# Optimization experiments

Hardware: AMD Instinct MI355X
Metric: run time of the kernel (lower is better)

Reference implementation:

```python
import jax, jax.numpy as jnp
import numpy as np

LATENT = 128
DISC = 64
RNN = 512
CODE = 512
INPUT = 2


def _lstm_cell(x, h, c, Wih, Whh, bih, bhh):
    # PyTorch LSTMCell: gate order (i, f, g, o)
    gates = x @ Wih.T + h @ Whh.T + bih + bhh
    i, f, g, o = jnp.split(gates, 4, axis=-1)
    c_new = jax.nn.sigmoid(f) * c + jax.nn.sigmoid(i) * jnp.tanh(g)
    h_new = jax.nn.sigmoid(o) * jnp.tanh(c_new)
    return h_new, c_new


def setup_inputs() -> dict:
    key = jax.random.key(0)
    ks = jax.random.split(key, 12)
    B = 4096
    s = lambda *sh: 1.0 / np.sqrt(sh[-1])
    inp = {
        'latent': jax.random.normal(ks[0], (B, LATENT), dtype=jnp.float32),
        'W_unpack': jax.random.normal(ks[1], (CODE, LATENT + INPUT), dtype=jnp.float32) * s(CODE, LATENT + INPUT),
        'b_unpack': jnp.zeros((CODE,), dtype=jnp.float32),
        'Wih0': jax.random.normal(ks[2], (4 * RNN, CODE), dtype=jnp.float32) * s(4 * RNN, CODE),
        'Whh0': jax.random.normal(ks[3], (4 * RNN, RNN), dtype=jnp.float32) * s(4 * RNN, RNN),
        'bih0': jnp.zeros((4 * RNN,), dtype=jnp.float32),
        'bhh0': jnp.zeros((4 * RNN,), dtype=jnp.float32),
        'Wih1': jax.random.normal(ks[4], (4 * RNN, RNN), dtype=jnp.float32) * s(4 * RNN, RNN),
        'Whh1': jax.random.normal(ks[5], (4 * RNN, RNN), dtype=jnp.float32) * s(4 * RNN, RNN),
        'bih1': jnp.zeros((4 * RNN,), dtype=jnp.float32),
        'bhh1': jnp.zeros((4 * RNN,), dtype=jnp.float32),
        'W_angle': jax.random.normal(ks[6], (DISC, RNN), dtype=jnp.float32) * s(DISC, RNN),
        'b_angle': jnp.zeros((DISC,), dtype=jnp.float32),
        'num_segments': 64,
    }
    return inp


def reference(latent, W_unpack, b_unpack, Wih0, Whh0, bih0, bhh0,
              Wih1, Whh1, bih1, bhh1, W_angle, b_angle, num_segments):
    B = latent.shape[0]
    space = jnp.linspace(-1.0, 1.0, DISC, dtype=latent.dtype)  # [DISC]
    # fixed gumbel noise for all steps: [S, B, DISC]
    u = jax.random.uniform(jax.random.key(42), (num_segments, B, DISC),
                           dtype=latent.dtype, minval=1e-8, maxval=1.0)
    gumbels = -jnp.log(-jnp.log(u))

    def step(carry, g):
        prev, h0, c0, h1, c1 = carry
        x = jnp.tanh(jnp.concatenate([latent, prev], axis=-1) @ W_unpack.T + b_unpack)
        h0, c0 = _lstm_cell(x, h0, c0, Wih0, Whh0, bih0, bhh0)
        h1, c1 = _lstm_cell(h0, h1, c1, Wih1, Whh1, bih1, bhh1)
        logits = h1 @ W_angle.T + b_angle
        # gumbel-softmax, tau=1 (torch default), hard=True with straight-through
        y_soft = jax.nn.softmax(logits + g, axis=-1)
        y_hard = jax.nn.one_hot(jnp.argmax(y_soft, axis=-1), DISC, dtype=y_soft.dtype)
        y = y_soft + jax.lax.stop_gradient(y_hard - y_soft)
        angles = jnp.sum(y * space, axis=-1, keepdims=True)  # [B,1]
        seg = jnp.concatenate([angles, jnp.zeros_like(angles)], axis=-1)  # [B,2]
        return (seg, h0, c0, h1, c1), seg

    z = jnp.zeros((B, RNN), dtype=latent.dtype)
    init = (jnp.zeros((B, INPUT), dtype=latent.dtype), z, z, z, z)
    _, segs = jax.lax.scan(step, init, gumbels)  # [S, B, 2]
    return jnp.transpose(segs, (1, 0, 2))  # [B, S, 2]
```

## Files before the change

kernel.cpp:

```cpp
#include <hip/hip_runtime.h>
#include <cstdint>

#define BATCH 4096
#define LATENT 128
#define RNN 512
#define CODE 512
#define DISC 64
#define NSEG 64
#define UNPACK_COLS 130

__device__ __forceinline__ uint32_t rotl32(uint32_t x, uint32_t r) {
  return (x << r) | (x >> (32u - r));
}

__device__ __forceinline__ uint32_t threefry_bits(uint32_t n) {
  const uint32_t k0 = 0u, k1 = 42u;
  const uint32_t ks2 = k0 ^ k1 ^ 0x1BD11BDAu;
  uint32_t x0 = 0u, x1 = n;
  x0 += k0; x1 += k1;
#define TF_ROUND(r) { x0 += x1; x1 = rotl32(x1, r); x1 ^= x0; }
  TF_ROUND(13) TF_ROUND(15) TF_ROUND(26) TF_ROUND(6)
  x0 += k1;  x1 += ks2 + 1u;
  TF_ROUND(17) TF_ROUND(29) TF_ROUND(16) TF_ROUND(24)
  x0 += ks2; x1 += k0 + 2u;
  TF_ROUND(13) TF_ROUND(15) TF_ROUND(26) TF_ROUND(6)
  x0 += k0;  x1 += k1 + 3u;
  TF_ROUND(17) TF_ROUND(29) TF_ROUND(16) TF_ROUND(24)
  x0 += k1;  x1 += ks2 + 4u;
  TF_ROUND(13) TF_ROUND(15) TF_ROUND(26) TF_ROUND(6)
  x0 += ks2; x1 += k0 + 5u;
#undef TF_ROUND
  return x0 ^ x1;
}

__global__ __launch_bounds__(256) void base_kernel(
    const float* __restrict__ latent, const float* __restrict__ Wu,
    const float* __restrict__ bu, float* __restrict__ base) {
  __shared__ float lrow[LATENT];
  const int b = blockIdx.x;
  if (threadIdx.x < LATENT) lrow[threadIdx.x] = latent[b * LATENT + threadIdx.x];
  __syncthreads();
  for (int n = threadIdx.x; n < CODE; n += 256) {
    const float* wr = Wu + (size_t)n * UNPACK_COLS;
    float acc = 0.f;
#pragma unroll 8
    for (int k = 0; k < LATENT; ++k) acc += lrow[k] * wr[k];
    base[(size_t)b * CODE + n] = acc + bu[n];
  }
}

__global__ __launch_bounds__(256) void x_kernel(
    const float* __restrict__ base, const float* __restrict__ angle,
    const float* __restrict__ Wu, float* __restrict__ xo) {
  const int idx = blockIdx.x * 256 + threadIdx.x;
  const int b = idx >> 9;
  const int n = idx & 511;
  xo[idx] = tanhf(base[idx] + angle[b] * Wu[(size_t)n * UNPACK_COLS + 128]);
}

#define BM 128
#define BN 128
#define BK 16

__global__ __launch_bounds__(256) void gemm_dual(
    const float* __restrict__ A1, const float* __restrict__ W1,
    const float* __restrict__ A2, const float* __restrict__ W2,
    const float* __restrict__ b1, const float* __restrict__ b2,
    float* __restrict__ C) {
  const int K = RNN;
  const int N = 4 * RNN;
  __shared__ __align__(16) float As[BK][BM];
  __shared__ __align__(16) float Ws[BK][BN];
  const int tid = threadIdx.x;
  const int tx = tid & 15, ty = tid >> 4;
  const int rowBase = blockIdx.y * BM;
  const int colBase = blockIdx.x * BN;
  const int lrow = tid >> 2;
  const int lk = (tid & 3) * 4;

  float acc[8][8];
#pragma unroll
  for (int i = 0; i < 8; ++i)
#pragma unroll
    for (int j = 0; j < 8; ++j) acc[i][j] = 0.f;

  for (int seg = 0; seg < 2; ++seg) {
    const float* __restrict__ A = seg ? A2 : A1;
    const float* __restrict__ W = seg ? W2 : W1;
    for (int k0 = 0; k0 < K; k0 += BK) {
      __syncthreads();
#pragma unroll
      for (int r = 0; r < 2; ++r) {
        const int rr = lrow + r * 64;
        float4 va = *(const float4*)&A[(size_t)(rowBase + rr) * K + k0 + lk];
        As[lk + 0][rr] = va.x; As[lk + 1][rr] = va.y;
        As[lk + 2][rr] = va.z; As[lk + 3][rr] = va.w;
        float4 vw = *(const float4*)&W[(size_t)(colBase + rr) * K + k0 + lk];
        Ws[lk + 0][rr] = vw.x; Ws[lk + 1][rr] = vw.y;
        Ws[lk + 2][rr] = vw.z; Ws[lk + 3][rr] = vw.w;
      }
      __syncthreads();
#pragma unroll
      for (int kk = 0; kk < BK; ++kk) {
        float4 a0 = *(const float4*)&As[kk][ty * 8];
        float4 a1 = *(const float4*)&As[kk][ty * 8 + 4];
        float4 w0 = *(const float4*)&Ws[kk][tx * 8];
        float4 w1 = *(const float4*)&Ws[kk][tx * 8 + 4];
        float av[8] = {a0.x, a0.y, a0.z, a0.w, a1.x, a1.y, a1.z, a1.w};
        float wv[8] = {w0.x, w0.y, w0.z, w0.w, w1.x, w1.y, w1.z, w1.w};
#pragma unroll
        for (int i = 0; i < 8; ++i)
#pragma unroll
          for (int j = 0; j < 8; ++j) acc[i][j] += av[i] * wv[j];
      }
    }
  }
#pragma unroll
  for (int i = 0; i < 8; ++i) {
    const int row = rowBase + ty * 8 + i;
#pragma unroll
    for (int j4 = 0; j4 < 2; ++j4) {
      const int col = colBase + tx * 8 + j4 * 4;
      float4 o;
      o.x = acc[i][j4 * 4 + 0] + b1[col + 0] + b2[col + 0];
      o.y = acc[i][j4 * 4 + 1] + b1[col + 1] + b2[col + 1];
      o.z = acc[i][j4 * 4 + 2] + b1[col + 2] + b2[col + 2];
      o.w = acc[i][j4 * 4 + 3] + b1[col + 3] + b2[col + 3];
      *(float4*)&C[(size_t)row * N + col] = o;
    }
  }
}

__device__ __forceinline__ float sigmoidf_(float v) {
  return 1.0f / (1.0f + expf(-v));
}

__global__ __launch_bounds__(256) void lstm_kernel(
    const float* __restrict__ gates, float* __restrict__ h, float* __restrict__ c) {
  const int idx = blockIdx.x * 256 + threadIdx.x;
  const int b = idx >> 9;
  const int j = idx & 511;
  const float* g = gates + (size_t)b * (4 * RNN);
  const float gi = g[j];
  const float gf = g[RNN + j];
  const float gg = g[2 * RNN + j];
  const float go = g[3 * RNN + j];
  const float cn = sigmoidf_(gf) * c[idx] + sigmoidf_(gi) * tanhf(gg);
  c[idx] = cn;
  h[idx] = sigmoidf_(go) * tanhf(cn);
}

__global__ __launch_bounds__(64) void head_kernel(
    const float* __restrict__ h1, const float* __restrict__ Wang,
    const float* __restrict__ bang, float* __restrict__ angle,
    float* __restrict__ out, int s) {
  const int b = blockIdx.x;
  const int d = threadIdx.x;
  const float4* hr = (const float4*)(h1 + (size_t)b * RNN);
  const float4* wr = (const float4*)(Wang + (size_t)d * RNN);
  float acc = 0.f;
#pragma unroll 16
  for (int k = 0; k < RNN / 4; ++k) {
    float4 a = hr[k], w = wr[k];
    acc += a.x * w.x; acc += a.y * w.y; acc += a.z * w.z; acc += a.w * w.w;
  }
  float z = acc + bang[d];
  const uint32_t n = ((uint32_t)s * BATCH + (uint32_t)b) * DISC + (uint32_t)d;
  const uint32_t bits = threefry_bits(n);
  const float f = __uint_as_float((bits >> 9) | 0x3f800000u) - 1.0f;
  const float u = fmaxf(1e-8f, f + 1e-8f);
  const float gum = -logf(-logf(u));
  z += gum;
  float m = z;
#pragma unroll
  for (int off = 32; off; off >>= 1) m = fmaxf(m, __shfl_xor(m, off));
  const float e = expf(z - m);
  float ssum = e;
#pragma unroll
  for (int off = 32; off; off >>= 1) ssum += __shfl_xor(ssum, off);
  const float y = e / ssum;
  float ymax = y;
#pragma unroll
  for (int off = 32; off; off >>= 1) ymax = fmaxf(ymax, __shfl_xor(ymax, off));
  const unsigned long long mask = __ballot(y == ymax);
  const int k = __ffsll(mask) - 1;
  if (d == 0) {
    const float sp = -1.0f + (2.0f / 63.0f) * (float)k;
    angle[b] = sp;
    out[((size_t)b * NSEG + s) * 2 + 0] = sp;
    out[((size_t)b * NSEG + s) * 2 + 1] = 0.0f;
  }
}

extern "C" void kernel_launch(void* const* d_in, const int* in_sizes, int n_in,
                              void* d_out, int out_size, void* d_ws, size_t ws_size,
                              hipStream_t stream) {
  const float* latent   = (const float*)d_in[0];
  const float* W_unpack = (const float*)d_in[1];
  const float* b_unpack = (const float*)d_in[2];
  const float* Wih0     = (const float*)d_in[3];
  const float* Whh0     = (const float*)d_in[4];
  const float* bih0     = (const float*)d_in[5];
  const float* bhh0     = (const float*)d_in[6];
  const float* Wih1     = (const float*)d_in[7];
  const float* Whh1     = (const float*)d_in[8];
  const float* bih1     = (const float*)d_in[9];
  const float* bhh1     = (const float*)d_in[10];
  const float* W_angle  = (const float*)d_in[11];
  const float* b_angle  = (const float*)d_in[12];
  float* out = (float*)d_out;

  float* ws    = (float*)d_ws;
  float* h0    = ws;
  float* c0    = h0 + (size_t)BATCH * RNN;
  float* h1    = c0 + (size_t)BATCH * RNN;
  float* c1    = h1 + (size_t)BATCH * RNN;
  float* angle = c1 + (size_t)BATCH * RNN;
  float* base  = angle + BATCH;
  float* x     = base + (size_t)BATCH * CODE;
  float* gates = x + (size_t)BATCH * CODE;

  hipMemsetAsync(ws, 0, ((size_t)4 * BATCH * RNN + BATCH) * sizeof(float), stream);

  base_kernel<<<BATCH, 256, 0, stream>>>(latent, W_unpack, b_unpack, base);

  dim3 ggrid((4 * RNN) / BN, BATCH / BM);
  for (int s = 0; s < NSEG; ++s) {
    x_kernel<<<(BATCH * CODE) / 256, 256, 0, stream>>>(base, angle, W_unpack, x);
    gemm_dual<<<ggrid, 256, 0, stream>>>(x, Wih0, h0, Whh0, bih0, bhh0, gates);
    lstm_kernel<<<(BATCH * RNN) / 256, 256, 0, stream>>>(gates, h0, c0);
    gemm_dual<<<ggrid, 256, 0, stream>>>(h0, Wih1, h1, Whh1, bih1, bhh1, gates);
    lstm_kernel<<<(BATCH * RNN) / 256, 256, 0, stream>>>(gates, h1, c1);
    head_kernel<<<BATCH, 64, 0, stream>>>(h1, W_angle, b_angle, angle, out, s);
  }
}
```

Before: 34.61 ms.

## Fuse LSTM cell pointwise update into gate GEMM epilogue with gate-interleaved tiles

The gate GEMM now loads weight rows so that each 128-column tile holds 32 hidden units for all four gates, letting the epilogue apply the LSTM cell update directly with a lane shuffle instead of writing a full gates tensor and launching a separate pointwise kernel. Hidden states are double-buffered across steps because the GEMM reads the old h while writing the new one. It also adds an XOR swizzle to the shared-memory tile layout to reduce bank conflicts. This removes the 4096x2048 gates round trip and two launches per step, at the cost of a more complex epilogue with some idle lanes.

```diff
diff --git a/kernel.cpp b/kernel.cpp
--- a/kernel.cpp
+++ b/kernel.cpp
@@ -33,6 +33,10 @@
   return x0 ^ x1;
 }
 
+__device__ __forceinline__ float sigmoidf_(float v) {
+  return 1.0f / (1.0f + expf(-v));
+}
+
 __global__ __launch_bounds__(256) void base_kernel(
     const float* __restrict__ latent, const float* __restrict__ Wu,
     const float* __restrict__ bu, float* __restrict__ base) {
@@ -62,21 +66,21 @@
 #define BN 128
 #define BK 16
 
-__global__ __launch_bounds__(256) void gemm_dual(
+__global__ __launch_bounds__(256) void gemm_lstm(
     const float* __restrict__ A1, const float* __restrict__ W1,
     const float* __restrict__ A2, const float* __restrict__ W2,
     const float* __restrict__ b1, const float* __restrict__ b2,
-    float* __restrict__ C) {
+    float* __restrict__ c_io, float* __restrict__ h_out) {
   const int K = RNN;
-  const int N = 4 * RNN;
   __shared__ __align__(16) float As[BK][BM];
   __shared__ __align__(16) float Ws[BK][BN];
   const int tid = threadIdx.x;
   const int tx = tid & 15, ty = tid >> 4;
+  const int bx = blockIdx.x;
   const int rowBase = blockIdx.y * BM;
-  const int colBase = blockIdx.x * BN;
   const int lrow = tid >> 2;
   const int lk = (tid & 3) * 4;
+  const int swz = (tid & 3) << 3;
 
   float acc[8][8];
 #pragma unroll
@@ -92,22 +96,25 @@
 #pragma unroll
       for (int r = 0; r < 2; ++r) {
         const int rr = lrow + r * 64;
-        float4 va = *(const float4*)&A[(size_t)(rowBase + rr) * K + k0 + lk];
-        As[lk + 0][rr] = va.x; As[lk + 1][rr] = va.y;
-        As[lk + 2][rr] = va.z; As[lk + 3][rr] = va.w;
-        float4 vw = *(const float4*)&W[(size_t)(colBase + rr) * K + k0 + lk];
-        Ws[lk + 0][rr] = vw.x; Ws[lk + 1][rr] = vw.y;
-        Ws[lk + 2][rr] = vw.z; Ws[lk + 3][rr] = vw.w;
+        const int cc = rr ^ swz;
+        const float4 va = *(const float4*)&A[(size_t)(rowBase + rr) * K + k0 + lk];
+        As[lk + 0][cc] = va.x; As[lk + 1][cc] = va.y;
+        As[lk + 2][cc] = va.z; As[lk + 3][cc] = va.w;
+        const int wn = ((rr >> 5) * RNN) + (bx << 5) + (rr & 31);
+        const float4 vw = *(const float4*)&W[(size_t)wn * K + k0 + lk];
+        Ws[lk + 0][cc] = vw.x; Ws[lk + 1][cc] = vw.y;
+        Ws[lk + 2][cc] = vw.z; Ws[lk + 3][cc] = vw.w;
       }
       __syncthreads();
 #pragma unroll
       for (int kk = 0; kk < BK; ++kk) {
-        float4 a0 = *(const float4*)&As[kk][ty * 8];
-        float4 a1 = *(const float4*)&As[kk][ty * 8 + 4];
-        float4 w0 = *(const float4*)&Ws[kk][tx * 8];
-        float4 w1 = *(const float4*)&Ws[kk][tx * 8 + 4];
-        float av[8] = {a0.x, a0.y, a0.z, a0.w, a1.x, a1.y, a1.z, a1.w};
-        float wv[8] = {w0.x, w0.y, w0.z, w0.w, w1.x, w1.y, w1.z, w1.w};
+        const int swk = (kk & 12) << 1;
+        const float4 a0 = *(const float4*)&As[kk][(ty * 4) ^ swk];
+        const float4 a1 = *(const float4*)&As[kk][(64 + ty * 4) ^ swk];
+        const float4 w0 = *(const float4*)&Ws[kk][(tx * 4) ^ swk];
+        const float4 w1 = *(const float4*)&Ws[kk][(64 + tx * 4) ^ swk];
+        const float av[8] = {a0.x, a0.y, a0.z, a0.w, a1.x, a1.y, a1.z, a1.w};
+        const float wv[8] = {w0.x, w0.y, w0.z, w0.w, w1.x, w1.y, w1.z, w1.w};
 #pragma unroll
         for (int i = 0; i < 8; ++i)
 #pragma unroll
@@ -115,39 +122,49 @@
       }
     }
   }
+
+  const int myjl = (tx & 7) * 4;
+  const int jbase = (bx << 5) + myjl;
+  const int g0 = (tx < 8) ? 0 : 1;
+  const int g1 = g0 + 2;
+  float bs0[4], bs1[4];
+#pragma unroll
+  for (int j = 0; j < 4; ++j) {
+    bs0[j] = b1[g0 * RNN + jbase + j] + b2[g0 * RNN + jbase + j];
+    bs1[j] = b1[g1 * RNN + jbase + j] + b2[g1 * RNN + jbase + j];
+  }
+  const bool low = (tx < 8);
 #pragma unroll
   for (int i = 0; i < 8; ++i) {
-    const int row = rowBase + ty * 8 + i;
-#pragma unroll
-    for (int j4 = 0; j4 < 2; ++j4) {
-      const int col = colBase + tx * 8 + j4 * 4;
-      float4 o;
-      o.x = acc[i][j4 * 4 + 0] + b1[col + 0] + b2[col + 0];
-      o.y = acc[i][j4 * 4 + 1] + b1[col + 1] + b2[col + 1];
-      o.z = acc[i][j4 * 4 + 2] + b1[col + 2] + b2[col + 2];
-      o.w = acc[i][j4 * 4 + 3] + b1[col + 3] + b2[col + 3];
-      *(float4*)&C[(size_t)row * N + col] = o;
+    float v0[4], v1[4], p0[4], p1[4];
+#pragma unroll
+    for (int j = 0; j < 4; ++j) {
+      v0[j] = acc[i][j] + bs0[j];
+      v1[j] = acc[i][4 + j] + bs1[j];
+      p0[j] = __shfl_xor(v0[j], 8);
+      p1[j] = __shfl_xor(v1[j], 8);
     }
-  }
-}
-
-__device__ __forceinline__ float sigmoidf_(float v) {
-  return 1.0f / (1.0f + expf(-v));
-}
-
-__global__ __launch_bounds__(256) void lstm_kernel(
-    const float* __restrict__ gates, float* __restrict__ h, float* __restrict__ c) {
-  const int idx = blockIdx.x * 256 + threadIdx.x;
-  const int b = idx >> 9;
-  const int j = idx & 511;
-  const float* g = gates + (size_t)b * (4 * RNN);
-  const float gi = g[j];
-  const float gf = g[RNN + j];
-  const float gg = g[2 * RNN + j];
-  const float go = g[3 * RNN + j];
-  const float cn = sigmoidf_(gf) * c[idx] + sigmoidf_(gi) * tanhf(gg);
-  c[idx] = cn;
-  h[idx] = sigmoidf_(go) * tanhf(cn);
+    const bool mine = low ? (i < 4) : (i >= 4);
+    if (mine) {
+      const int row = rowBase + (low ? (ty * 4 + i) : (64 + ty * 4 + (i - 4)));
+      const size_t off = (size_t)row * RNN + jbase;
+      const float4 cold = *(const float4*)&c_io[off];
+      const float co[4] = {cold.x, cold.y, cold.z, cold.w};
+      float cn[4], hn[4];
+#pragma unroll
+      for (int j = 0; j < 4; ++j) {
+        const float fi = low ? v0[j] : p0[j];
+        const float fg = low ? v1[j] : p1[j];
+        const float ff = low ? p0[j] : v0[j];
+        const float fo = low ? p1[j] : v1[j];
+        const float c2 = sigmoidf_(ff) * co[j] + sigmoidf_(fi) * tanhf(fg);
+        cn[j] = c2;
+        hn[j] = sigmoidf_(fo) * tanhf(c2);
+      }
+      *(float4*)&c_io[off] = make_float4(cn[0], cn[1], cn[2], cn[3]);
+      *(float4*)&h_out[off] = make_float4(hn[0], hn[1], hn[2], hn[3]);
+    }
+  }
 }
 
 __global__ __launch_bounds__(64) void head_kernel(
@@ -210,27 +227,30 @@
   const float* b_angle  = (const float*)d_in[12];
   float* out = (float*)d_out;
 
+  const size_t HC = (size_t)BATCH * RNN;
   float* ws    = (float*)d_ws;
-  float* h0    = ws;
-  float* c0    = h0 + (size_t)BATCH * RNN;
-  float* h1    = c0 + (size_t)BATCH * RNN;
-  float* c1    = h1 + (size_t)BATCH * RNN;
-  float* angle = c1 + (size_t)BATCH * RNN;
-  float* base  = angle + BATCH;
-  float* x     = base + (size_t)BATCH * CODE;
-  float* gates = x + (size_t)BATCH * CODE;
-
-  hipMemsetAsync(ws, 0, ((size_t)4 * BATCH * RNN + BATCH) * sizeof(float), stream);
+  float* h0a   = ws;
+  float* h1a   = h0a + HC;
+  float* c0    = h1a + HC;
+  float* c1    = c0 + HC;
+  float* angle = c1 + HC;
+  float* h0b   = angle + BATCH;
+  float* h1b   = h0b + HC;
+  float* x     = h1b + HC;
+  float* base  = x + (size_t)BATCH * CODE;
+
+  hipMemsetAsync(ws, 0, (4 * HC + BATCH) * sizeof(float), stream);
 
   base_kernel<<<BATCH, 256, 0, stream>>>(latent, W_unpack, b_unpack, base);
 
-  dim3 ggrid((4 * RNN) / BN, BATCH / BM);
+  dim3 ggrid(16, 32);
   for (int s = 0; s < NSEG; ++s) {
+    const int p = s & 1;
+    float* h0p = p ? h0b : h0a; float* h0n = p ? h0a : h0b;
+    float* h1p = p ? h1b : h1a; float* h1n = p ? h1a : h1b;
     x_kernel<<<(BATCH * CODE) / 256, 256, 0, stream>>>(base, angle, W_unpack, x);
-    gemm_dual<<<ggrid, 256, 0, stream>>>(x, Wih0, h0, Whh0, bih0, bhh0, gates);
-    lstm_kernel<<<(BATCH * RNN) / 256, 256, 0, stream>>>(gates, h0, c0);
-    gemm_dual<<<ggrid, 256, 0, stream>>>(h0, Wih1, h1, Whh1, bih1, bhh1, gates);
-    lstm_kernel<<<(BATCH * RNN) / 256, 256, 0, stream>>>(gates, h1, c1);
-    head_kernel<<<BATCH, 64, 0, stream>>>(h1, W_angle, b_angle, angle, out, s);
-  }
-}
+    gemm_lstm<<<ggrid, 256, 0, stream>>>(x, Wih0, h0p, Whh0, bih0, bhh0, c0, h0n);
+    gemm_lstm<<<ggrid, 256, 0, stream>>>(h0n, Wih1, h1p, Whh1, bih1, bhh1, c1, h1n);
+    head_kernel<<<BATCH, 64, 0, stream>>>(h1n, W_angle, b_angle, angle, out, s);
+  }
+}
```

Result: faster. 33.79 ms (-2.4%).
